# Performance work log

Hardware: AMD Instinct MI355X
Metric: run time of the kernel (lower is better)

## Reference

```python
import jax, jax.numpy as jnp
import numpy as np

DIM, HEADS = 128, 8
DH = DIM // HEADS
SCALE = DH ** -0.5
N, E = 50000, 800000


def setup_inputs() -> dict:
    key = jax.random.key(0)
    ks = jax.random.split(key, 12)
    w = lambda k: jax.random.normal(k, (DIM, DIM), dtype=jnp.float32) * 0.02
    b = lambda k: jax.random.normal(k, (DIM,), dtype=jnp.float32) * 0.02
    return {
        "q_nodes": jax.random.normal(ks[0], (N, DIM), dtype=jnp.float32),
        "k_edges": jax.random.normal(ks[1], (E, DIM), dtype=jnp.float32),
        "v_edges": jax.random.normal(ks[2], (E, DIM), dtype=jnp.float32),
        "edge_index": jax.random.randint(ks[3], (2, E), 0, N, dtype=jnp.int64),
        "Wq": w(ks[4]), "bq": b(ks[5]),
        "Wk": w(ks[6]), "bk": b(ks[7]),
        "Wv": w(ks[8]), "bv": b(ks[9]),
        "Wo": w(ks[10]), "bo": b(ks[11]),
    }


def reference(q_nodes, k_edges, v_edges, edge_index, Wq, bq, Wk, bk, Wv, bv, Wo, bo):
    n, e = q_nodes.shape[0], k_edges.shape[0]
    dst = edge_index[0]  # src (edge_index[1]) is unused by the module
    q = (q_nodes @ Wq.T + bq).reshape(n, HEADS, DH)
    k = (k_edges @ Wk.T + bk).reshape(e, HEADS, DH)
    v = (v_edges @ Wv.T + bv).reshape(e, HEADS, DH)
    # per-edge score: dot(q[dst], k) per head -> [E, H]
    score = jnp.einsum('ehd,ehd->eh', q[dst], k) * SCALE
    # segment (per-dst-node) softmax over edges, numerically stable
    m = jax.ops.segment_max(score, dst, num_segments=n)          # [N, H]
    ex = jnp.exp(score - m[dst])                                  # [E, H]
    s = jax.ops.segment_sum(ex, dst, num_segments=n)             # [N, H]
    w = ex / (s[dst] + 1e-16)                                     # [E, H]
    weighted_v = (v * w[..., None]).reshape(e, DIM)               # [E, dim]
    aggr = jax.ops.segment_sum(weighted_v, dst, num_segments=n)  # [N, dim]
    return aggr @ Wo.T + bo
```

## Files before the change

### kernel.cpp

```cpp
#include <hip/hip_runtime.h>

#define TM 64
#define NTHREADS 256
#define PAD 132

typedef __attribute__((ext_vector_type(8))) short short8;
typedef __attribute__((ext_vector_type(4))) float f32x4;

__device__ __forceinline__ short f2bf(float f) {
  union { float f; unsigned u; } uf; uf.f = f;
  unsigned r = uf.u + 0x7FFFu + ((uf.u >> 16) & 1u);
  return (short)(r >> 16);
}
__device__ __forceinline__ float bf2f(short s) {
  union { unsigned u; float f; } uf; uf.u = ((unsigned)(unsigned short)s) << 16;
  return uf.f;
}
__device__ __forceinline__ short8 pack8(float4 a, float4 b) {
  short8 r;
  r[0] = f2bf(a.x); r[1] = f2bf(a.y); r[2] = f2bf(a.z); r[3] = f2bf(a.w);
  r[4] = f2bf(b.x); r[5] = f2bf(b.y); r[6] = f2bf(b.z); r[7] = f2bf(b.w);
  return r;
}


__global__ __launch_bounds__(512) void proj_mfma(
    const float* __restrict__ X, const short* __restrict__ Wb,
    const float* __restrict__ bias, float* __restrict__ Y, int M, float scale) {
  __shared__ short Xb[8192];
  int t = threadIdx.x;
  int w = t >> 6, l = t & 63, g = l >> 4, c = l & 15;
  short8 wf[4];
#pragma unroll
  for (int kc = 0; kc < 4; ++kc)
    wf[kc] = *(const short8*)(Wb + (w * 16 + c) * 128 + kc * 32 + g * 8);
  float4 b4 = *(const float4*)(bias + w * 16 + g * 4);

  for (int rb = blockIdx.x * 64; rb < M; rb += gridDim.x * 64) {
    {
      int r = t >> 3, q8 = t & 7;
      int row = rb + r; if (row >= M) row = M - 1;
      const float4* xs = (const float4*)(X + (size_t)row * 128 + q8 * 16);
      float4 x0 = xs[0], x1 = xs[1], x2 = xs[2], x3 = xs[3];
      int sw = (r & 7) << 4;
      *(short8*)((char*)Xb + r * 256 + ((q8 * 32) ^ sw)) = pack8(x0, x1);
      *(short8*)((char*)Xb + r * 256 + ((q8 * 32 + 16) ^ sw)) = pack8(x2, x3);
    }
    __syncthreads();
#pragma unroll
    for (int et = 0; et < 4; ++et) {
      int rl = et * 16 + c;
      f32x4 acc = {};
      int sw = (rl & 7) << 4;
#pragma unroll
      for (int kc = 0; kc < 4; ++kc) {
        short8 xb = *(const short8*)((char*)Xb + rl * 256 + ((kc * 64 + g * 16) ^ sw));
        acc = __builtin_amdgcn_mfma_f32_16x16x32_bf16(wf[kc], xb, acc, 0, 0, 0);
      }
      int row = rb + rl;
      if (row < M) {
        float4 o;
        o.x = (acc[0] + b4.x) * scale; o.y = (acc[1] + b4.y) * scale;
        o.z = (acc[2] + b4.z) * scale; o.w = (acc[3] + b4.w) * scale;
        *(float4*)(Y + (size_t)row * 128 + w * 16 + g * 4) = o;
      }
    }
    __syncthreads();
  }
}


__global__ __launch_bounds__(256) void hist_kernel(const int* __restrict__ dst,
                                                   int* __restrict__ cnt, int E) {
  int e = blockIdx.x * 256 + threadIdx.x;
  if (e < E) atomicAdd(&cnt[dst[e]], 1);
}

__global__ __launch_bounds__(1024) void scan_part(const int* __restrict__ cnt,
                                                  int* __restrict__ part, int N) {
  __shared__ int ws[16];
  int t = threadIdx.x, i = blockIdx.x * 1024 + t;
  int v = (i < N) ? cnt[i] : 0;
#pragma unroll
  for (int d = 1; d < 64; d <<= 1) v += __shfl_xor(v, d);
  if ((t & 63) == 0) ws[t >> 6] = v;
  __syncthreads();
  if (t < 16) {
    int x = ws[t];
#pragma unroll
    for (int d = 1; d < 16; d <<= 1) x += __shfl_xor(x, d);
    if (t == 0) part[blockIdx.x] = x;
  }
}

__global__ __launch_bounds__(64) void scan_offs(int* __restrict__ part, int P) {
  int t = threadIdx.x;
  int carry = 0;
  for (int base = 0; base < P; base += 64) {
    int i = base + t;
    int v = (i < P) ? part[i] : 0;
    int x = v;
#pragma unroll
    for (int d = 1; d < 64; d <<= 1) { int y = __shfl_up(x, d); if (t >= d) x += y; }
    if (i < P) part[i] = x - v + carry;
    carry += __shfl(x, 63);
  }
}

__global__ __launch_bounds__(1024) void scan_final(const int* __restrict__ cnt,
                                                   const int* __restrict__ part,
                                                   int* __restrict__ rp,
                                                   int* __restrict__ cur, int N) {
  __shared__ int ws[16];
  __shared__ int wofs[16];
  int t = threadIdx.x, i = blockIdx.x * 1024 + t;
  int lane = t & 63, wid = t >> 6;
  int v = (i < N) ? cnt[i] : 0;
  int x = v;
#pragma unroll
  for (int d = 1; d < 64; d <<= 1) { int y = __shfl_up(x, d); if (lane >= d) x += y; }
  if (lane == 63) ws[wid] = x;
  __syncthreads();
  if (t == 0) {
    int s = 0;
#pragma unroll
    for (int k2 = 0; k2 < 16; ++k2) { int tmp = ws[k2]; wofs[k2] = s; s += tmp; }
  }
  __syncthreads();
  int incl = x + wofs[wid] + part[blockIdx.x];
  int excl = incl - v;
  if (i < N) {
    rp[i] = excl; cur[i] = excl;
    if (i == N - 1) rp[N] = incl;
  }
}

__global__ __launch_bounds__(256) void scatter_kernel(const int* __restrict__ dst,
                                                      int* __restrict__ cursor,
                                                      int* __restrict__ edge_ids, int E) {
  int e = blockIdx.x * 256 + threadIdx.x;
  if (e < E) {
    int p = atomicAdd(&cursor[dst[e]], 1);
    edge_ids[p] = e;
  }
}

__global__ __launch_bounds__(256) void wprep4(
    const float* __restrict__ Wq, const float* __restrict__ Wk,
    const float* __restrict__ Wv, const float* __restrict__ Wo,
    short* __restrict__ wqb, short* __restrict__ wkb,
    short* __restrict__ wvb, short* __restrict__ wob) {
  int i = blockIdx.x * 256 + threadIdx.x;
  if (i < 16384) {
    wqb[i] = f2bf(Wq[i]); wkb[i] = f2bf(Wk[i]);
    wvb[i] = f2bf(Wv[i]); wob[i] = f2bf(Wo[i]);
  }
}


__global__ __launch_bounds__(512) void edge_mfma3(
    const float* __restrict__ K, const float* __restrict__ V,
    const int* __restrict__ dst,
    const short* __restrict__ wkb, const short* __restrict__ wvb,
    const float* __restrict__ bk, const float* __restrict__ qp,
    float* __restrict__ exb, short* __restrict__ wv, int E) {
  __shared__ short Kb[8192];
  __shared__ short Vb[8192];
  __shared__ float exs[512];
  int t = threadIdx.x;
  int w = t >> 6, l = t & 63, g = l >> 4, c = l & 15;
  short8 wK[4], wV[4];
#pragma unroll
  for (int kc = 0; kc < 4; ++kc) {
    wK[kc] = *(const short8*)(wkb + (w * 16 + c) * 128 + kc * 32 + g * 8);
    wV[kc] = *(const short8*)(wvb + (w * 16 + c) * 128 + kc * 32 + g * 8);
  }
  float4 bk4 = *(const float4*)(bk + w * 16 + g * 4);

  int r = t >> 3, q8 = t & 7;
  int sw_st = (r & 7) << 4;
  int b0 = r * 256 + ((q8 * 32) ^ sw_st);
  int b1 = r * 256 + ((q8 * 32 + 16) ^ sw_st);
  int stride = gridDim.x * 64;

  int eb = blockIdx.x * 64;

  float4 k0, k1, k2, k3;
  float4 qv[4];
  {
    int row0 = eb + r; if (row0 >= E) row0 = E - 1;
    const float4* ks = (const float4*)(K + (size_t)row0 * 128 + q8 * 16);
    k0 = ks[0]; k1 = ks[1]; k2 = ks[2]; k3 = ks[3];
    int d0[4];
#pragma unroll
    for (int et = 0; et < 4; ++et) {
      int e = eb + et * 16 + c; if (e >= E) e = E - 1;
      d0[et] = dst[e];
    }
#pragma unroll
    for (int et = 0; et < 4; ++et)
      qv[et] = *(const float4*)(qp + (size_t)d0[et] * 128 + w * 16 + g * 4);
  }

  for (; eb < E; eb += stride) {
    int ebn = eb + stride;
    bool has_next = ebn < E;

    __syncthreads();
    *(short8*)((char*)Kb + b0) = pack8(k0, k1);
    *(short8*)((char*)Kb + b1) = pack8(k2, k3);
    float4 v0, v1, v2, v3;
    {
      int rowv = eb + r; if (rowv >= E) rowv = E - 1;
      const float4* vs = (const float4*)(V + (size_t)rowv * 128 + q8 * 16);
      v0 = vs[0]; v1 = vs[1]; v2 = vs[2]; v3 = vs[3];
    }
    int dn[4];
    if (has_next) {
#pragma unroll
      for (int et = 0; et < 4; ++et) {
        int e = ebn + et * 16 + c; if (e >= E) e = E - 1;
        dn[et] = dst[e];
      }
    }
    __syncthreads();

    float ex[4];
#pragma unroll
    for (int et = 0; et < 4; ++et) {
      int eloc = et * 16 + c;
      int swr = (eloc & 7) << 4;
      f32x4 acc = {};
#pragma unroll
      for (int kc = 0; kc < 4; ++kc) {
        short8 xb = *(const short8*)((char*)Kb + eloc * 256 + ((kc * 64 + g * 16) ^ swr));
        acc = __builtin_amdgcn_mfma_f32_16x16x32_bf16(wK[kc], xb, acc, 0, 0, 0);
      }
      float s = (acc[0] + bk4.x) * qv[et].x + (acc[1] + bk4.y) * qv[et].y +
                (acc[2] + bk4.z) * qv[et].z + (acc[3] + bk4.w) * qv[et].w;
      s += __shfl_xor(s, 16);
      s += __shfl_xor(s, 32);
      ex[et] = __expf(s);
      if (g == 0) exs[eloc * 8 + w] = ex[et];
    }

    *(short8*)((char*)Vb + b0) = pack8(v0, v1);
    *(short8*)((char*)Vb + b1) = pack8(v2, v3);
    if (has_next) {
      int rowk = ebn + r; if (rowk >= E) rowk = E - 1;
      const float4* ks = (const float4*)(K + (size_t)rowk * 128 + q8 * 16);
      k0 = ks[0]; k1 = ks[1]; k2 = ks[2]; k3 = ks[3];
#pragma unroll
      for (int et = 0; et < 4; ++et)
        qv[et] = *(const float4*)(qp + (size_t)dn[et] * 128 + w * 16 + g * 4);
    }
    __syncthreads();

#pragma unroll
    for (int et = 0; et < 4; ++et) {
      int eloc = et * 16 + c;
      int swr = (eloc & 7) << 4;
      f32x4 acc = {};
#pragma unroll
      for (int kc = 0; kc < 4; ++kc) {
        short8 xb = *(const short8*)((char*)Vb + eloc * 256 + ((kc * 64 + g * 16) ^ swr));
        acc = __builtin_amdgcn_mfma_f32_16x16x32_bf16(wV[kc], xb, acc, 0, 0, 0);
      }
      short4 sv;
      sv.x = f2bf(acc[0] * ex[et]); sv.y = f2bf(acc[1] * ex[et]);
      sv.z = f2bf(acc[2] * ex[et]); sv.w = f2bf(acc[3] * ex[et]);
      *(short4*)((char*)Kb + eloc * 256 + ((w * 32 + g * 8) ^ swr)) = sv;
    }
    __syncthreads();

    {
      int row = eb + r;
      if (row < E) {
        short8 a = *(const short8*)((char*)Kb + r * 256 + ((q8 * 32) ^ sw_st));
        short8 b = *(const short8*)((char*)Kb + r * 256 + ((q8 * 32 + 16) ^ sw_st));
        *(short8*)(wv + (size_t)row * 128 + q8 * 16) = a;
        *(short8*)(wv + (size_t)row * 128 + q8 * 16 + 8) = b;
      }
      if (t < 128) {
        int r2 = t >> 1, half = t & 1;
        int row2 = eb + r2;
        if (row2 < E)
          *(float4*)(exb + (size_t)row2 * 8 + half * 4) = *(const float4*)(&exs[r2 * 8 + half * 4]);
      }
    }
  }
}


__global__ __launch_bounds__(256) void pull2(
    const short* __restrict__ wv, const float* __restrict__ exb,
    const int* __restrict__ eid, const int* __restrict__ rp,
    const float* __restrict__ bv, float* __restrict__ aggr, int N) {
  int w = threadIdx.x >> 6, l = threadIdx.x & 63;
  int n = blockIdx.x * 4 + w;
  if (n >= N) return;
  int beg = rp[n], end = rp[n + 1];
  int h = l >> 3;
  float a0 = 0.f, a1 = 0.f, s = 0.f;
  int j = beg;
  for (; j + 1 < end; j += 2) {
    int e0 = eid[j], e1 = eid[j + 1];
    unsigned v0 = *(const unsigned*)(wv + (size_t)e0 * 128 + l * 2);
    unsigned v1 = *(const unsigned*)(wv + (size_t)e1 * 128 + l * 2);
    float s0 = exb[(size_t)e0 * 8 + h], s1 = exb[(size_t)e1 * 8 + h];
    a0 += bf2f((short)(v0 & 0xFFFFu)) + bf2f((short)(v1 & 0xFFFFu));
    a1 += bf2f((short)(v0 >> 16)) + bf2f((short)(v1 >> 16));
    s += s0 + s1;
  }
  if (j < end) {
    int e0 = eid[j];
    unsigned v0 = *(const unsigned*)(wv + (size_t)e0 * 128 + l * 2);
    s += exb[(size_t)e0 * 8 + h];
    a0 += bf2f((short)(v0 & 0xFFFFu));
    a1 += bf2f((short)(v0 >> 16));
  }
  float2 o;
  if (end > beg) {
    float inv = 1.f / (s + 1e-16f);
    float2 bvv = *(const float2*)(bv + l * 2);
    o.x = a0 * inv + bvv.x; o.y = a1 * inv + bvv.y;
  } else {
    o.x = 0.f; o.y = 0.f;
  }
  *(float2*)(aggr + (size_t)n * 128 + l * 2) = o;
}


__device__ __forceinline__ void stage_x(float (*Xs)[PAD], const float* __restrict__ X,
                                        int rowbase, int M, int t) {
#pragma unroll
  for (int i = 0; i < 8; ++i) {
    int idx = t + NTHREADS * i;
    int r = idx >> 5, q = idx & 31;
    int row = rowbase + r;
    if (row >= M) row = M - 1;
    const float4 v = *(const float4*)(X + (size_t)row * 128 + q * 4);
    *(float4*)(&Xs[r][q * 4]) = v;
  }
}

__device__ __forceinline__ void gemm_tile(const float (*Xs)[PAD], float (*WT)[PAD],
                                          const float* __restrict__ W,
                                          float acc[8][4], int r0, int c0, int t) {
#pragma unroll 1
  for (int kk = 0; kk < 128; kk += 32) {
    {
      int j = t >> 1, half = t & 1;
      const float* src = W + j * 128 + kk + half * 16;
      float4 a = *(const float4*)(src);
      float4 b = *(const float4*)(src + 4);
      float4 c = *(const float4*)(src + 8);
      float4 d = *(const float4*)(src + 12);
      int cb = half * 16;
      WT[cb + 0][j] = a.x;  WT[cb + 1][j] = a.y;  WT[cb + 2][j] = a.z;  WT[cb + 3][j] = a.w;
      WT[cb + 4][j] = b.x;  WT[cb + 5][j] = b.y;  WT[cb + 6][j] = b.z;  WT[cb + 7][j] = b.w;
      WT[cb + 8][j] = c.x;  WT[cb + 9][j] = c.y;  WT[cb + 10][j] = c.z; WT[cb + 11][j] = c.w;
      WT[cb + 12][j] = d.x; WT[cb + 13][j] = d.y; WT[cb + 14][j] = d.z; WT[cb + 15][j] = d.w;
    }
    __syncthreads();
#pragma unroll
    for (int c2 = 0; c2 < 16; ++c2) {
      float4 wa = *(const float4*)(&WT[2 * c2][c0]);
      float4 wb = *(const float4*)(&WT[2 * c2 + 1][c0]);
#pragma unroll
      for (int i = 0; i < 8; ++i) {
        float2 xv = *(const float2*)(&Xs[r0 + i][kk + 2 * c2]);
        acc[i][0] = fmaf(xv.x, wa.x, acc[i][0]);
        acc[i][1] = fmaf(xv.x, wa.y, acc[i][1]);
        acc[i][2] = fmaf(xv.x, wa.z, acc[i][2]);
        acc[i][3] = fmaf(xv.x, wa.w, acc[i][3]);
        acc[i][0] = fmaf(xv.y, wb.x, acc[i][0]);
        acc[i][1] = fmaf(xv.y, wb.y, acc[i][1]);
        acc[i][2] = fmaf(xv.y, wb.z, acc[i][2]);
        acc[i][3] = fmaf(xv.y, wb.w, acc[i][3]);
      }
    }
    __syncthreads();
  }
}

__global__ __launch_bounds__(NTHREADS) void proj_kernel(
    const float* __restrict__ X, const float* __restrict__ W,
    const float* __restrict__ b, float* __restrict__ Y, int M) {
  __shared__ float Xs[TM][PAD];
  __shared__ float WT[32][PAD];
  int t = threadIdx.x;
  int B0 = blockIdx.x * TM;
  stage_x(Xs, X, B0, M, t);
  __syncthreads();
  int r0 = (t >> 5) * 8, m = t & 31, c0 = m * 4;
  float acc[8][4] = {};
  gemm_tile(Xs, WT, W, acc, r0, c0, t);
  float4 bv = ((const float4*)b)[m];
#pragma unroll
  for (int i = 0; i < 8; ++i) {
    int row = B0 + r0 + i;
    if (row < M) {
      float4 o;
      o.x = acc[i][0] + bv.x; o.y = acc[i][1] + bv.y;
      o.z = acc[i][2] + bv.z; o.w = acc[i][3] + bv.w;
      *(float4*)(Y + (size_t)row * 128 + c0) = o;
    }
  }
}

__global__ __launch_bounds__(NTHREADS) void edge_kernel(
    const float* __restrict__ Kin, const float* __restrict__ Vin,
    const int* __restrict__ eidx,
    const float* __restrict__ Wk, const float* __restrict__ bk,
    const float* __restrict__ Wv, const float* __restrict__ bv,
    const float* __restrict__ qp, float* __restrict__ s_sum,
    float* __restrict__ aggr, int E) {
  __shared__ float Xs[TM][PAD];
  __shared__ float WT[32][PAD];
  __shared__ int dsts[TM];
  int t = threadIdx.x;
  int e0 = blockIdx.x * TM;
  if (t < TM) {
    int idx = e0 + t;
    if (idx >= E) idx = E - 1;
    dsts[t] = eidx[idx];
  }
  stage_x(Xs, Kin, e0, E, t);
  __syncthreads();
  int r0 = (t >> 5) * 8, m = t & 31, c0 = m * 4;
  int h = m >> 2;
  float acc[8][4] = {};
  gemm_tile(Xs, WT, Wk, acc, r0, c0, t);
  float4 bkv = ((const float4*)bk)[m];
  float ex[8];
#pragma unroll
  for (int i = 0; i < 8; ++i) {
    int r = r0 + i;
    const float4 qv = *(const float4*)(qp + (size_t)dsts[r] * 128 + c0);
    float p = (acc[i][0] + bkv.x) * qv.x + (acc[i][1] + bkv.y) * qv.y +
              (acc[i][2] + bkv.z) * qv.z + (acc[i][3] + bkv.w) * qv.w;
    p += __shfl_xor(p, 1);
    p += __shfl_xor(p, 2);
    float e = __expf(p * 0.25f);
    ex[i] = e;
    if ((m & 3) == 0 && (e0 + r) < E)
      atomicAdd(&s_sum[(size_t)dsts[r] * 8 + h], e);
  }
  __syncthreads();
  stage_x(Xs, Vin, e0, E, t);
  __syncthreads();
#pragma unroll
  for (int i = 0; i < 8; ++i)
#pragma unroll
    for (int j = 0; j < 4; ++j) acc[i][j] = 0.f;
  gemm_tile(Xs, WT, Wv, acc, r0, c0, t);
  float4 bvv = ((const float4*)bv)[m];
#pragma unroll
  for (int i = 0; i < 8; ++i) {
    int r = r0 + i;
    if ((e0 + r) < E) {
      size_t base = (size_t)dsts[r] * 128 + c0;
      atomicAdd(&aggr[base + 0], (acc[i][0] + bvv.x) * ex[i]);
      atomicAdd(&aggr[base + 1], (acc[i][1] + bvv.y) * ex[i]);
      atomicAdd(&aggr[base + 2], (acc[i][2] + bvv.z) * ex[i]);
      atomicAdd(&aggr[base + 3], (acc[i][3] + bvv.w) * ex[i]);
    }
  }
}

__global__ __launch_bounds__(NTHREADS) void out_kernel(
    const float* __restrict__ aggr, const float* __restrict__ s_sum,
    const float* __restrict__ W, const float* __restrict__ b,
    float* __restrict__ Y, int M) {
  __shared__ float Xs[TM][PAD];
  __shared__ float WT[32][PAD];
  int t = threadIdx.x;
  int B0 = blockIdx.x * TM;
#pragma unroll
  for (int i = 0; i < 8; ++i) {
    int idx = t + NTHREADS * i;
    int r = idx >> 5, q = idx & 31;
    int row = B0 + r;
    if (row >= M) row = M - 1;
    float4 v = *(const float4*)(aggr + (size_t)row * 128 + q * 4);
    float inv = 1.0f / (s_sum[(size_t)row * 8 + (q >> 2)] + 1e-16f);
    v.x *= inv; v.y *= inv; v.z *= inv; v.w *= inv;
    *(float4*)(&Xs[r][q * 4]) = v;
  }
  __syncthreads();
  int r0 = (t >> 5) * 8, m = t & 31, c0 = m * 4;
  float acc[8][4] = {};
  gemm_tile(Xs, WT, W, acc, r0, c0, t);
  float4 bv = ((const float4*)b)[m];
#pragma unroll
  for (int i = 0; i < 8; ++i) {
    int row = B0 + r0 + i;
    if (row < M) {
      float4 o;
      o.x = acc[i][0] + bv.x; o.y = acc[i][1] + bv.y;
      o.z = acc[i][2] + bv.z; o.w = acc[i][3] + bv.w;
      *(float4*)(Y + (size_t)row * 128 + c0) = o;
    }
  }
}


extern "C" void kernel_launch(void* const* d_in, const int* in_sizes, int n_in,
                              void* d_out, int out_size, void* d_ws, size_t ws_size,
                              hipStream_t stream) {
  const float* q_nodes = (const float*)d_in[0];
  const float* k_edges = (const float*)d_in[1];
  const float* v_edges = (const float*)d_in[2];
  const int* eidx = (const int*)d_in[3];
  const float* Wq = (const float*)d_in[4];
  const float* bq = (const float*)d_in[5];
  const float* Wk = (const float*)d_in[6];
  const float* bk = (const float*)d_in[7];
  const float* Wv = (const float*)d_in[8];
  const float* bv = (const float*)d_in[9];
  const float* Wo = (const float*)d_in[10];
  const float* bo = (const float*)d_in[11];

  int N = in_sizes[0] / 128;
  int E = in_sizes[1] / 128;
  int P = (N + 1023) / 1024;

  size_t off = 0;
  auto alloc = [&](size_t b) { size_t o = off; off += (b + 255) & ~(size_t)255; return o; };
  size_t o_qp   = alloc((size_t)N * 128 * 4);
  size_t o_aggr = alloc((size_t)N * 128 * 4);
  size_t o_exb  = alloc((size_t)E * 8 * 4);
  size_t o_rp   = alloc(((size_t)N + 1) * 4);
  size_t o_cur  = alloc((size_t)N * 4);
  size_t o_cnt  = alloc((size_t)N * 4);
  size_t o_eid  = alloc((size_t)E * 4);
  size_t o_part = alloc((size_t)(P + 1) * 4);
  size_t o_wqb  = alloc((size_t)16384 * 2);
  size_t o_wkb  = alloc((size_t)16384 * 2);
  size_t o_wvb  = alloc((size_t)16384 * 2);
  size_t o_wob  = alloc((size_t)16384 * 2);
  size_t o_wv   = alloc((size_t)E * 128 * 2);

  if (off <= ws_size) {
    char* base = (char*)d_ws;
    float* qp    = (float*)(base + o_qp);
    float* aggr  = (float*)(base + o_aggr);
    float* exb   = (float*)(base + o_exb);
    int*   rp    = (int*)(base + o_rp);
    int*   cur   = (int*)(base + o_cur);
    int*   cnt   = (int*)(base + o_cnt);
    int*   eid   = (int*)(base + o_eid);
    int*   part  = (int*)(base + o_part);
    short* wqb   = (short*)(base + o_wqb);
    short* wkb   = (short*)(base + o_wkb);
    short* wvb   = (short*)(base + o_wvb);
    short* wob   = (short*)(base + o_wob);
    short* wvbuf = (short*)(base + o_wv);

    hipMemsetAsync(cnt, 0, (size_t)N * 4, stream);
    wprep4<<<64, 256, 0, stream>>>(Wq, Wk, Wv, Wo, wqb, wkb, wvb, wob);
    proj_mfma<<<(N + 63) / 64, 512, 0, stream>>>(q_nodes, wqb, bq, qp, N, 0.25f);
    hist_kernel<<<(E + 255) / 256, 256, 0, stream>>>(eidx, cnt, E);
    scan_part<<<P, 1024, 0, stream>>>(cnt, part, N);
    scan_offs<<<1, 64, 0, stream>>>(part, P);
    scan_final<<<P, 1024, 0, stream>>>(cnt, part, rp, cur, N);
    scatter_kernel<<<(E + 255) / 256, 256, 0, stream>>>(eidx, cur, eid, E);
    int eblk = (E + 63) / 64; if (eblk > 1024) eblk = 1024;
    edge_mfma3<<<eblk, 512, 0, stream>>>(k_edges, v_edges, eidx, wkb, wvb, bk, qp,
                                         exb, wvbuf, E);
    pull2<<<(N + 3) / 4, 256, 0, stream>>>(wvbuf, exb, eid, rp, bv, aggr, N);
    proj_mfma<<<(N + 63) / 64, 512, 0, stream>>>(aggr, wob, bo, (float*)d_out, N, 1.0f);
  } else {
    float* q_proj = (float*)d_ws;
    float* s_sum  = q_proj + (size_t)N * 128;
    float* aggr   = s_sum + (size_t)N * 8;
    hipMemsetAsync(s_sum, 0, (size_t)N * 136 * sizeof(float), stream);
    int nblk = (N + TM - 1) / TM;
    int eblk = (E + TM - 1) / TM;
    proj_kernel<<<nblk, NTHREADS, 0, stream>>>(q_nodes, Wq, bq, q_proj, N);
    edge_kernel<<<eblk, NTHREADS, 0, stream>>>(k_edges, v_edges, eidx, Wk, bk, Wv, bv,
                                               q_proj, s_sum, aggr, E);
    out_kernel<<<nblk, NTHREADS, 0, stream>>>(aggr, s_sum, Wo, bo, (float*)d_out, N);
  }
}
```

Before: 448.5 us.

## Write edge outputs in dst-sorted order and split K/V edge kernel

The scatter now records each edge's destination-sorted slot (perm) instead of an edge-id list. The edge kernels write exp-scores and weighted V rows directly into sorted positions, so the pull kernel reads contiguous rows without indirection. The fused K/V edge kernel is split into a score kernel and a V-projection kernel, which adds a second pass that re-reads exb via perm. The scattered global writes replace the previous gathered reads.

Measured after the change: 448.9 us. No clear change (+0.1%).

```diff
diff --git a/kernel.cpp b/kernel.cpp
--- a/kernel.cpp
+++ b/kernel.cpp
@@ -135,14 +135,11 @@
   }
 }
 
-__global__ __launch_bounds__(256) void scatter_kernel(const int* __restrict__ dst,
-                                                      int* __restrict__ cursor,
-                                                      int* __restrict__ edge_ids, int E) {
+__global__ __launch_bounds__(256) void perm_kernel(const int* __restrict__ dst,
+                                                   int* __restrict__ cursor,
+                                                   int* __restrict__ perm, int E) {
   int e = blockIdx.x * 256 + threadIdx.x;
-  if (e < E) {
-    int p = atomicAdd(&cursor[dst[e]], 1);
-    edge_ids[p] = e;
-  }
+  if (e < E) perm[e] = atomicAdd(&cursor[dst[e]], 1);
 }
 
 __global__ __launch_bounds__(256) void wprep4(
@@ -158,74 +155,62 @@
 }
 
 
-__global__ __launch_bounds__(512) void edge_mfma3(
-    const float* __restrict__ K, const float* __restrict__ V,
-    const int* __restrict__ dst,
-    const short* __restrict__ wkb, const short* __restrict__ wvb,
+__global__ __launch_bounds__(512) void kproj_score(
+    const float* __restrict__ K, const int* __restrict__ eidx,
+    const int* __restrict__ perm, const short* __restrict__ wkb,
     const float* __restrict__ bk, const float* __restrict__ qp,
-    float* __restrict__ exb, short* __restrict__ wv, int E) {
+    float* __restrict__ exb, int E) {
   __shared__ short Kb[8192];
-  __shared__ short Vb[8192];
-  __shared__ float exs[512];
   int t = threadIdx.x;
   int w = t >> 6, l = t & 63, g = l >> 4, c = l & 15;
-  short8 wK[4], wV[4];
-#pragma unroll
-  for (int kc = 0; kc < 4; ++kc) {
+  short8 wK[4];
+#pragma unroll
+  for (int kc = 0; kc < 4; ++kc)
     wK[kc] = *(const short8*)(wkb + (w * 16 + c) * 128 + kc * 32 + g * 8);
-    wV[kc] = *(const short8*)(wvb + (w * 16 + c) * 128 + kc * 32 + g * 8);
-  }
   float4 bk4 = *(const float4*)(bk + w * 16 + g * 4);
-
   int r = t >> 3, q8 = t & 7;
-  int sw_st = (r & 7) << 4;
-  int b0 = r * 256 + ((q8 * 32) ^ sw_st);
-  int b1 = r * 256 + ((q8 * 32 + 16) ^ sw_st);
+  int b0 = r * 256 + ((q8 * 32) ^ ((r & 7) << 4));
   int stride = gridDim.x * 64;
-
   int eb = blockIdx.x * 64;
 
   float4 k0, k1, k2, k3;
-  float4 qv[4];
+  int d[4], p[4];
   {
     int row0 = eb + r; if (row0 >= E) row0 = E - 1;
     const float4* ks = (const float4*)(K + (size_t)row0 * 128 + q8 * 16);
     k0 = ks[0]; k1 = ks[1]; k2 = ks[2]; k3 = ks[3];
-    int d0[4];
 #pragma unroll
     for (int et = 0; et < 4; ++et) {
       int e = eb + et * 16 + c; if (e >= E) e = E - 1;
-      d0[et] = dst[e];
-    }
-#pragma unroll
-    for (int et = 0; et < 4; ++et)
-      qv[et] = *(const float4*)(qp + (size_t)d0[et] * 128 + w * 16 + g * 4);
+      d[et] = eidx[e]; p[et] = perm[e];
+    }
   }
 
   for (; eb < E; eb += stride) {
     int ebn = eb + stride;
-    bool has_next = ebn < E;
-
+    bool hn = ebn < E;
     __syncthreads();
     *(short8*)((char*)Kb + b0) = pack8(k0, k1);
-    *(short8*)((char*)Kb + b1) = pack8(k2, k3);
-    float4 v0, v1, v2, v3;
-    {
-      int rowv = eb + r; if (rowv >= E) rowv = E - 1;
-      const float4* vs = (const float4*)(V + (size_t)rowv * 128 + q8 * 16);
-      v0 = vs[0]; v1 = vs[1]; v2 = vs[2]; v3 = vs[3];
-    }
-    int dn[4];
-    if (has_next) {
+    *(short8*)((char*)Kb + (b0 ^ 16)) = pack8(k2, k3);
+    float4 qv[4];
+#pragma unroll
+    for (int et = 0; et < 4; ++et)
+      qv[et] = *(const float4*)(qp + (size_t)d[et] * 128 + w * 16 + g * 4);
+    if (hn) {
+      int rowk = ebn + r; if (rowk >= E) rowk = E - 1;
+      const float4* ks = (const float4*)(K + (size_t)rowk * 128 + q8 * 16);
+      k0 = ks[0]; k1 = ks[1]; k2 = ks[2]; k3 = ks[3];
+    }
+    int dn[4], pn[4];
+    if (hn) {
 #pragma unroll
       for (int et = 0; et < 4; ++et) {
         int e = ebn + et * 16 + c; if (e >= E) e = E - 1;
-        dn[et] = dst[e];
+        dn[et] = eidx[e]; pn[et] = perm[e];
       }
     }
     __syncthreads();
 
-    float ex[4];
 #pragma unroll
     for (int et = 0; et < 4; ++et) {
       int eloc = et * 16 + c;
@@ -240,19 +225,70 @@
                 (acc[2] + bk4.z) * qv[et].z + (acc[3] + bk4.w) * qv[et].w;
       s += __shfl_xor(s, 16);
       s += __shfl_xor(s, 32);
-      ex[et] = __expf(s);
-      if (g == 0) exs[eloc * 8 + w] = ex[et];
-    }
-
+      if (g == 0) exb[(size_t)p[et] * 8 + w] = __expf(s);
+    }
+    if (hn) {
+#pragma unroll
+      for (int et = 0; et < 4; ++et) { d[et] = dn[et]; p[et] = pn[et]; }
+    }
+  }
+}
+
+
+__global__ __launch_bounds__(512) void vproj_weight(
+    const float* __restrict__ V, const int* __restrict__ perm,
+    const short* __restrict__ wvb, const float* __restrict__ exb,
+    short* __restrict__ wv, int E) {
+  __shared__ short Vb[8192];
+  __shared__ short Ob[8192];
+  int t = threadIdx.x;
+  int w = t >> 6, l = t & 63, g = l >> 4, c = l & 15;
+  short8 wV[4];
+#pragma unroll
+  for (int kc = 0; kc < 4; ++kc)
+    wV[kc] = *(const short8*)(wvb + (w * 16 + c) * 128 + kc * 32 + g * 8);
+  int r = t >> 3, q8 = t & 7;
+  int b0 = r * 256 + ((q8 * 32) ^ ((r & 7) << 4));
+  int stride = gridDim.x * 64;
+  int eb = blockIdx.x * 64;
+
+  float4 v0, v1, v2, v3;
+  int p[4];
+  {
+    int row0 = eb + r; if (row0 >= E) row0 = E - 1;
+    const float4* vs = (const float4*)(V + (size_t)row0 * 128 + q8 * 16);
+    v0 = vs[0]; v1 = vs[1]; v2 = vs[2]; v3 = vs[3];
+#pragma unroll
+    for (int et = 0; et < 4; ++et) {
+      int e = eb + et * 16 + c; if (e >= E) e = E - 1;
+      p[et] = perm[e];
+    }
+  }
+
+  for (; eb < E; eb += stride) {
+    int ebn = eb + stride;
+    bool hn = ebn < E;
+    __syncthreads();
     *(short8*)((char*)Vb + b0) = pack8(v0, v1);
-    *(short8*)((char*)Vb + b1) = pack8(v2, v3);
-    if (has_next) {
-      int rowk = ebn + r; if (rowk >= E) rowk = E - 1;
-      const float4* ks = (const float4*)(K + (size_t)rowk * 128 + q8 * 16);
-      k0 = ks[0]; k1 = ks[1]; k2 = ks[2]; k3 = ks[3];
-#pragma unroll
-      for (int et = 0; et < 4; ++et)
-        qv[et] = *(const float4*)(qp + (size_t)dn[et] * 128 + w * 16 + g * 4);
+    *(short8*)((char*)Vb + (b0 ^ 16)) = pack8(v2, v3);
+    float ev[4];
+#pragma unroll
+    for (int et = 0; et < 4; ++et)
+      ev[et] = exb[(size_t)p[et] * 8 + w];
+    int erow = eb + r; if (erow >= E) erow = E - 1;
+    int prow = perm[erow];
+    if (hn) {
+      int rowv = ebn + r; if (rowv >= E) rowv = E - 1;
+      const float4* vs = (const float4*)(V + (size_t)rowv * 128 + q8 * 16);
+      v0 = vs[0]; v1 = vs[1]; v2 = vs[2]; v3 = vs[3];
+    }
+    int pn[4];
+    if (hn) {
+#pragma unroll
+      for (int et = 0; et < 4; ++et) {
+        int e = ebn + et * 16 + c; if (e >= E) e = E - 1;
+        pn[et] = perm[e];
+      }
     }
     __syncthreads();
 
@@ -267,35 +303,31 @@
         acc = __builtin_amdgcn_mfma_f32_16x16x32_bf16(wV[kc], xb, acc, 0, 0, 0);
       }
       short4 sv;
-      sv.x = f2bf(acc[0] * ex[et]); sv.y = f2bf(acc[1] * ex[et]);
-      sv.z = f2bf(acc[2] * ex[et]); sv.w = f2bf(acc[3] * ex[et]);
-      *(short4*)((char*)Kb + eloc * 256 + ((w * 32 + g * 8) ^ swr)) = sv;
+      sv.x = f2bf(acc[0] * ev[et]); sv.y = f2bf(acc[1] * ev[et]);
+      sv.z = f2bf(acc[2] * ev[et]); sv.w = f2bf(acc[3] * ev[et]);
+      *(short4*)((char*)Ob + eloc * 256 + ((w * 32 + g * 8) ^ swr)) = sv;
     }
     __syncthreads();
 
     {
-      int row = eb + r;
-      if (row < E) {
-        short8 a = *(const short8*)((char*)Kb + r * 256 + ((q8 * 32) ^ sw_st));
-        short8 b = *(const short8*)((char*)Kb + r * 256 + ((q8 * 32 + 16) ^ sw_st));
-        *(short8*)(wv + (size_t)row * 128 + q8 * 16) = a;
-        *(short8*)(wv + (size_t)row * 128 + q8 * 16 + 8) = b;
-      }
-      if (t < 128) {
-        int r2 = t >> 1, half = t & 1;
-        int row2 = eb + r2;
-        if (row2 < E)
-          *(float4*)(exb + (size_t)row2 * 8 + half * 4) = *(const float4*)(&exs[r2 * 8 + half * 4]);
-      }
-    }
-  }
-}
-
-
-__global__ __launch_bounds__(256) void pull2(
+      int sw = (r & 7) << 4;
+      short8 a = *(const short8*)((char*)Ob + r * 256 + ((q8 * 32) ^ sw));
+      short8 b = *(const short8*)((char*)Ob + r * 256 + ((q8 * 32 + 16) ^ sw));
+      *(short8*)(wv + (size_t)prow * 128 + q8 * 16) = a;
+      *(short8*)(wv + (size_t)prow * 128 + q8 * 16 + 8) = b;
+    }
+    if (hn) {
+#pragma unroll
+      for (int et = 0; et < 4; ++et) p[et] = pn[et];
+    }
+  }
+}
+
+
+__global__ __launch_bounds__(256) void pull3(
     const short* __restrict__ wv, const float* __restrict__ exb,
-    const int* __restrict__ eid, const int* __restrict__ rp,
-    const float* __restrict__ bv, float* __restrict__ aggr, int N) {
+    const int* __restrict__ rp, const float* __restrict__ bv,
+    float* __restrict__ aggr, int N) {
   int w = threadIdx.x >> 6, l = threadIdx.x & 63;
   int n = blockIdx.x * 4 + w;
   if (n >= N) return;
@@ -304,20 +336,18 @@
   float a0 = 0.f, a1 = 0.f, s = 0.f;
   int j = beg;
   for (; j + 1 < end; j += 2) {
-    int e0 = eid[j], e1 = eid[j + 1];
-    unsigned v0 = *(const unsigned*)(wv + (size_t)e0 * 128 + l * 2);
-    unsigned v1 = *(const unsigned*)(wv + (size_t)e1 * 128 + l * 2);
-    float s0 = exb[(size_t)e0 * 8 + h], s1 = exb[(size_t)e1 * 8 + h];
-    a0 += bf2f((short)(v0 & 0xFFFFu)) + bf2f((short)(v1 & 0xFFFFu));
-    a1 += bf2f((short)(v0 >> 16)) + bf2f((short)(v1 >> 16));
+    unsigned u0 = *(const unsigned*)(wv + (size_t)j * 128 + l * 2);
+    unsigned u1 = *(const unsigned*)(wv + (size_t)(j + 1) * 128 + l * 2);
+    float s0 = exb[(size_t)j * 8 + h], s1 = exb[(size_t)(j + 1) * 8 + h];
+    a0 += bf2f((short)(u0 & 0xFFFFu)) + bf2f((short)(u1 & 0xFFFFu));
+    a1 += bf2f((short)(u0 >> 16)) + bf2f((short)(u1 >> 16));
     s += s0 + s1;
   }
   if (j < end) {
-    int e0 = eid[j];
-    unsigned v0 = *(const unsigned*)(wv + (size_t)e0 * 128 + l * 2);
-    s += exb[(size_t)e0 * 8 + h];
-    a0 += bf2f((short)(v0 & 0xFFFFu));
-    a1 += bf2f((short)(v0 >> 16));
+    unsigned u0 = *(const unsigned*)(wv + (size_t)j * 128 + l * 2);
+    s += exb[(size_t)j * 8 + h];
+    a0 += bf2f((short)(u0 & 0xFFFFu));
+    a1 += bf2f((short)(u0 >> 16));
   }
   float2 o;
   if (end > beg) {
@@ -534,7 +564,7 @@
   size_t o_rp   = alloc(((size_t)N + 1) * 4);
   size_t o_cur  = alloc((size_t)N * 4);
   size_t o_cnt  = alloc((size_t)N * 4);
-  size_t o_eid  = alloc((size_t)E * 4);
+  size_t o_perm = alloc((size_t)E * 4);
   size_t o_part = alloc((size_t)(P + 1) * 4);
   size_t o_wqb  = alloc((size_t)16384 * 2);
   size_t o_wkb  = alloc((size_t)16384 * 2);
@@ -550,7 +580,7 @@
     int*   rp    = (int*)(base + o_rp);
     int*   cur   = (int*)(base + o_cur);
     int*   cnt   = (int*)(base + o_cnt);
-    int*   eid   = (int*)(base + o_eid);
+    int*   perm  = (int*)(base + o_perm);
     int*   part  = (int*)(base + o_part);
     short* wqb   = (short*)(base + o_wqb);
     short* wkb   = (short*)(base + o_wkb);
@@ -565,11 +595,12 @@
     scan_part<<<P, 1024, 0, stream>>>(cnt, part, N);
     scan_offs<<<1, 64, 0, stream>>>(part, P);
     scan_final<<<P, 1024, 0, stream>>>(cnt, part, rp, cur, N);
-    scatter_kernel<<<(E + 255) / 256, 256, 0, stream>>>(eidx, cur, eid, E);
+    perm_kernel<<<(E + 255) / 256, 256, 0, stream>>>(eidx, cur, perm, E);
+
     int eblk = (E + 63) / 64; if (eblk > 1024) eblk = 1024;
-    edge_mfma3<<<eblk, 512, 0, stream>>>(k_edges, v_edges, eidx, wkb, wvb, bk, qp,
-                                         exb, wvbuf, E);
-    pull2<<<(N + 3) / 4, 256, 0, stream>>>(wvbuf, exb, eid, rp, bv, aggr, N);
+    kproj_score<<<eblk, 512, 0, stream>>>(k_edges, eidx, perm, wkb, bk, qp, exb, E);
+    vproj_weight<<<eblk, 512, 0, stream>>>(v_edges, perm, wvb, exb, wvbuf, E);
+    pull3<<<(N + 3) / 4, 256, 0, stream>>>(wvbuf, exb, rp, bv, aggr, N);
     proj_mfma<<<(N + 63) / 64, 512, 0, stream>>>(aggr, wob, bo, (float*)d_out, N, 1.0f);
   } else {
     float* q_proj = (float*)d_ws;
```

## Scatter edge outputs into CSR order so the pull pass reads contiguously

Applied to the files above, without the earlier changes.

The scatter kernel now records each edge's destination slot (a permutation) instead of an edge-id list. The edge kernel writes the weighted-V rows and exp scores straight to those sorted slots, so the pull kernel reads contiguous memory per node without indirection through eid. The cost of random access moves from gathered reads in the pull kernel to scattered 256-byte row writes in the edge kernel.

Measured after the change: 428.8 us. -4.4%, faster.

```diff
diff --git a/kernel.cpp b/kernel.cpp
--- a/kernel.cpp
+++ b/kernel.cpp
@@ -135,14 +135,11 @@
   }
 }
 
-__global__ __launch_bounds__(256) void scatter_kernel(const int* __restrict__ dst,
-                                                      int* __restrict__ cursor,
-                                                      int* __restrict__ edge_ids, int E) {
+__global__ __launch_bounds__(256) void perm_kernel(const int* __restrict__ dst,
+                                                   int* __restrict__ cursor,
+                                                   int* __restrict__ perm, int E) {
   int e = blockIdx.x * 256 + threadIdx.x;
-  if (e < E) {
-    int p = atomicAdd(&cursor[dst[e]], 1);
-    edge_ids[p] = e;
-  }
+  if (e < E) perm[e] = atomicAdd(&cursor[dst[e]], 1);
 }
 
 __global__ __launch_bounds__(256) void wprep4(
@@ -158,15 +155,16 @@
 }
 
 
-__global__ __launch_bounds__(512) void edge_mfma3(
+__global__ __launch_bounds__(512) void edge_mfma4(
     const float* __restrict__ K, const float* __restrict__ V,
-    const int* __restrict__ dst,
+    const int* __restrict__ eidx, const int* __restrict__ perm,
     const short* __restrict__ wkb, const short* __restrict__ wvb,
     const float* __restrict__ bk, const float* __restrict__ qp,
     float* __restrict__ exb, short* __restrict__ wv, int E) {
   __shared__ short Kb[8192];
   __shared__ short Vb[8192];
   __shared__ float exs[512];
+  __shared__ int sh_perm[64];
   int t = threadIdx.x;
   int w = t >> 6, l = t & 63, g = l >> 4, c = l & 15;
   short8 wK[4], wV[4];
@@ -180,22 +178,22 @@
   int r = t >> 3, q8 = t & 7;
   int sw_st = (r & 7) << 4;
   int b0 = r * 256 + ((q8 * 32) ^ sw_st);
-  int b1 = r * 256 + ((q8 * 32 + 16) ^ sw_st);
   int stride = gridDim.x * 64;
-
   int eb = blockIdx.x * 64;
 
   float4 k0, k1, k2, k3;
   float4 qv[4];
+  int prm_r;
   {
     int row0 = eb + r; if (row0 >= E) row0 = E - 1;
     const float4* ks = (const float4*)(K + (size_t)row0 * 128 + q8 * 16);
     k0 = ks[0]; k1 = ks[1]; k2 = ks[2]; k3 = ks[3];
+    prm_r = perm[row0];
     int d0[4];
 #pragma unroll
     for (int et = 0; et < 4; ++et) {
       int e = eb + et * 16 + c; if (e >= E) e = E - 1;
-      d0[et] = dst[e];
+      d0[et] = eidx[e];
     }
 #pragma unroll
     for (int et = 0; et < 4; ++et)
@@ -204,23 +202,26 @@
 
   for (; eb < E; eb += stride) {
     int ebn = eb + stride;
-    bool has_next = ebn < E;
+    bool hn = ebn < E;
 
     __syncthreads();
     *(short8*)((char*)Kb + b0) = pack8(k0, k1);
-    *(short8*)((char*)Kb + b1) = pack8(k2, k3);
+    *(short8*)((char*)Kb + (b0 ^ 16)) = pack8(k2, k3);
+    if (q8 == 0) sh_perm[r] = prm_r;
     float4 v0, v1, v2, v3;
     {
       int rowv = eb + r; if (rowv >= E) rowv = E - 1;
       const float4* vs = (const float4*)(V + (size_t)rowv * 128 + q8 * 16);
       v0 = vs[0]; v1 = vs[1]; v2 = vs[2]; v3 = vs[3];
     }
-    int dn[4];
-    if (has_next) {
+    int dn[4], prm_rn = 0;
+    if (hn) {
+      int rowk = ebn + r; if (rowk >= E) rowk = E - 1;
+      prm_rn = perm[rowk];
 #pragma unroll
       for (int et = 0; et < 4; ++et) {
         int e = ebn + et * 16 + c; if (e >= E) e = E - 1;
-        dn[et] = dst[e];
+        dn[et] = eidx[e];
       }
     }
     __syncthreads();
@@ -245,8 +246,8 @@
     }
 
     *(short8*)((char*)Vb + b0) = pack8(v0, v1);
-    *(short8*)((char*)Vb + b1) = pack8(v2, v3);
-    if (has_next) {
+    *(short8*)((char*)Vb + (b0 ^ 16)) = pack8(v2, v3);
+    if (hn) {
       int rowk = ebn + r; if (rowk >= E) rowk = E - 1;
       const float4* ks = (const float4*)(K + (size_t)rowk * 128 + q8 * 16);
       k0 = ks[0]; k1 = ks[1]; k2 = ks[2]; k3 = ks[3];
@@ -276,26 +277,30 @@
     {
       int row = eb + r;
       if (row < E) {
+        int slot = sh_perm[r];
         short8 a = *(const short8*)((char*)Kb + r * 256 + ((q8 * 32) ^ sw_st));
         short8 b = *(const short8*)((char*)Kb + r * 256 + ((q8 * 32 + 16) ^ sw_st));
-        *(short8*)(wv + (size_t)row * 128 + q8 * 16) = a;
-        *(short8*)(wv + (size_t)row * 128 + q8 * 16 + 8) = b;
+        *(short8*)(wv + (size_t)slot * 128 + q8 * 16) = a;
+        *(short8*)(wv + (size_t)slot * 128 + q8 * 16 + 8) = b;
       }
       if (t < 128) {
         int r2 = t >> 1, half = t & 1;
-        int row2 = eb + r2;
-        if (row2 < E)
-          *(float4*)(exb + (size_t)row2 * 8 + half * 4) = *(const float4*)(&exs[r2 * 8 + half * 4]);
-      }
-    }
-  }
-}
-
-
-__global__ __launch_bounds__(256) void pull2(
+        if (eb + r2 < E) {
+          int slot2 = sh_perm[r2];
+          *(float4*)(exb + (size_t)slot2 * 8 + half * 4) =
+              *(const float4*)(&exs[r2 * 8 + half * 4]);
+        }
+      }
+    }
+    prm_r = prm_rn;
+  }
+}
+
+
+__global__ __launch_bounds__(256) void pull3(
     const short* __restrict__ wv, const float* __restrict__ exb,
-    const int* __restrict__ eid, const int* __restrict__ rp,
-    const float* __restrict__ bv, float* __restrict__ aggr, int N) {
+    const int* __restrict__ rp, const float* __restrict__ bv,
+    float* __restrict__ aggr, int N) {
   int w = threadIdx.x >> 6, l = threadIdx.x & 63;
   int n = blockIdx.x * 4 + w;
   if (n >= N) return;
@@ -304,20 +309,18 @@
   float a0 = 0.f, a1 = 0.f, s = 0.f;
   int j = beg;
   for (; j + 1 < end; j += 2) {
-    int e0 = eid[j], e1 = eid[j + 1];
-    unsigned v0 = *(const unsigned*)(wv + (size_t)e0 * 128 + l * 2);
-    unsigned v1 = *(const unsigned*)(wv + (size_t)e1 * 128 + l * 2);
-    float s0 = exb[(size_t)e0 * 8 + h], s1 = exb[(size_t)e1 * 8 + h];
-    a0 += bf2f((short)(v0 & 0xFFFFu)) + bf2f((short)(v1 & 0xFFFFu));
-    a1 += bf2f((short)(v0 >> 16)) + bf2f((short)(v1 >> 16));
+    unsigned u0 = *(const unsigned*)(wv + (size_t)j * 128 + l * 2);
+    unsigned u1 = *(const unsigned*)(wv + (size_t)(j + 1) * 128 + l * 2);
+    float s0 = exb[(size_t)j * 8 + h], s1 = exb[(size_t)(j + 1) * 8 + h];
+    a0 += bf2f((short)(u0 & 0xFFFFu)) + bf2f((short)(u1 & 0xFFFFu));
+    a1 += bf2f((short)(u0 >> 16)) + bf2f((short)(u1 >> 16));
     s += s0 + s1;
   }
   if (j < end) {
-    int e0 = eid[j];
-    unsigned v0 = *(const unsigned*)(wv + (size_t)e0 * 128 + l * 2);
-    s += exb[(size_t)e0 * 8 + h];
-    a0 += bf2f((short)(v0 & 0xFFFFu));
-    a1 += bf2f((short)(v0 >> 16));
+    unsigned u0 = *(const unsigned*)(wv + (size_t)j * 128 + l * 2);
+    s += exb[(size_t)j * 8 + h];
+    a0 += bf2f((short)(u0 & 0xFFFFu));
+    a1 += bf2f((short)(u0 >> 16));
   }
   float2 o;
   if (end > beg) {
@@ -534,7 +537,7 @@
   size_t o_rp   = alloc(((size_t)N + 1) * 4);
   size_t o_cur  = alloc((size_t)N * 4);
   size_t o_cnt  = alloc((size_t)N * 4);
-  size_t o_eid  = alloc((size_t)E * 4);
+  size_t o_perm = alloc((size_t)E * 4);
   size_t o_part = alloc((size_t)(P + 1) * 4);
   size_t o_wqb  = alloc((size_t)16384 * 2);
   size_t o_wkb  = alloc((size_t)16384 * 2);
@@ -550,7 +553,7 @@
     int*   rp    = (int*)(base + o_rp);
     int*   cur   = (int*)(base + o_cur);
     int*   cnt   = (int*)(base + o_cnt);
-    int*   eid   = (int*)(base + o_eid);
+    int*   perm  = (int*)(base + o_perm);
     int*   part  = (int*)(base + o_part);
     short* wqb   = (short*)(base + o_wqb);
     short* wkb   = (short*)(base + o_wkb);
@@ -565,11 +568,12 @@
     scan_part<<<P, 1024, 0, stream>>>(cnt, part, N);
     scan_offs<<<1, 64, 0, stream>>>(part, P);
     scan_final<<<P, 1024, 0, stream>>>(cnt, part, rp, cur, N);
-    scatter_kernel<<<(E + 255) / 256, 256, 0, stream>>>(eidx, cur, eid, E);
+    perm_kernel<<<(E + 255) / 256, 256, 0, stream>>>(eidx, cur, perm, E);
+
     int eblk = (E + 63) / 64; if (eblk > 1024) eblk = 1024;
-    edge_mfma3<<<eblk, 512, 0, stream>>>(k_edges, v_edges, eidx, wkb, wvb, bk, qp,
-                                         exb, wvbuf, E);
-    pull2<<<(N + 3) / 4, 256, 0, stream>>>(wvbuf, exb, eid, rp, bv, aggr, N);
+    edge_mfma4<<<eblk, 512, 0, stream>>>(k_edges, v_edges, eidx, perm, wkb, wvb,
+                                         bk, qp, exb, wvbuf, E);
+    pull3<<<(N + 3) / 4, 256, 0, stream>>>(wvbuf, exb, rp, bv, aggr, N);
     proj_mfma<<<(N + 63) / 64, 512, 0, stream>>>(aggr, wob, bo, (float*)d_out, N, 1.0f);
   } else {
     float* q_proj = (float*)d_ws;
```
